# Performance work log

Hardware: AMD Instinct MI355X
Metric: run time of the kernel (lower is better)

The kernel has to match this reference:

```python
import jax, jax.numpy as jnp
import numpy as np

D_MODEL = 512
H = 8
DK = D_MODEL // H  # 64


def setup_inputs() -> dict:
    key = jax.random.key(0)
    ks = jax.random.split(key, 8)
    B, S = 2, 4096
    q = jax.random.normal(ks[0], (B, S, D_MODEL), dtype=jnp.float32)
    k = jax.random.normal(ks[1], (B, S, D_MODEL), dtype=jnp.float32)
    v = jax.random.normal(ks[2], (B, S, D_MODEL), dtype=jnp.float32)
    # per-head projection weights, torch nn.Linear layout [out, in], stacked over heads
    scale = 1.0 / np.sqrt(D_MODEL)
    Wq = jax.random.uniform(ks[3], (H, DK, D_MODEL), jnp.float32, -scale, scale)
    Wk = jax.random.uniform(ks[4], (H, DK, D_MODEL), jnp.float32, -scale, scale)
    Wv = jax.random.uniform(ks[5], (H, DK, D_MODEL), jnp.float32, -scale, scale)
    Wo = jax.random.uniform(ks[6], (D_MODEL, D_MODEL), jnp.float32, -scale, scale)
    # causal mask (True = keep), matches masked_fill(mask.logical_not(), -inf)
    mask = jnp.tril(jnp.ones((S, S), dtype=jnp.bool_))
    return {"q": q, "k": k, "v": v, "Wq": Wq, "Wk": Wk, "Wv": Wv, "Wo": Wo, "mask": mask}


def reference(q, k, v, Wq, Wk, Wv, Wo, mask):
    # per-head projections (stacked): x @ W^T for each head -> [B, H, S, DK]
    qh = jnp.einsum('bsd,hed->bhse', q, Wq)
    kh = jnp.einsum('bsd,hed->bhse', k, Wk)
    vh = jnp.einsum('bsd,hed->bhse', v, Wv)
    scaling = 1.0 / np.sqrt(DK)
    scores = jnp.einsum('bhse,bhte->bhst', qh, kh) * scaling  # [B,H,S,S]
    scores = jnp.where(mask, scores, -jnp.inf)
    attn = jax.nn.softmax(scores, axis=-1)
    heads = jnp.einsum('bhst,bhte->bhse', attn, vh)  # [B,H,S,DK]
    B, _, S, _ = heads.shape
    concat = jnp.transpose(heads, (0, 2, 1, 3)).reshape(B, S, D_MODEL)
    return concat @ Wo.T
```

## Files before the change

kernel.cpp:

```cpp
#include <hip/hip_runtime.h>
#include <hip/hip_bf16.h>
#include <math.h>

typedef __bf16 bf16_t;
typedef __bf16 bf16x8 __attribute__((ext_vector_type(8)));
typedef __bf16 bf16x4 __attribute__((ext_vector_type(4)));
typedef short short4v __attribute__((ext_vector_type(4)));
typedef float f32x4 __attribute__((ext_vector_type(4)));

__device__ __forceinline__ f32x4 mfma_k32(bf16x8 a, bf16x8 b, f32x4 c) {
    return __builtin_amdgcn_mfma_f32_16x16x32_bf16(a, b, c, 0, 0, 0);
}

__device__ __forceinline__ f32x4 mfma_k16(bf16x4 a, bf16x4 b, f32x4 c) {
#if __has_builtin(__builtin_amdgcn_mfma_f32_16x16x16_bf16)
    return __builtin_amdgcn_mfma_f32_16x16x16_bf16(a, b, c, 0, 0, 0);
#elif __has_builtin(__builtin_amdgcn_mfma_f32_16x16x16bf16_1k)
    short4v as, bs;
    __builtin_memcpy(&as, &a, 8);
    __builtin_memcpy(&bs, &b, 8);
    return __builtin_amdgcn_mfma_f32_16x16x16bf16_1k(as, bs, c, 0, 0, 0);
#else
    f32x4 d = c;
    asm volatile("v_mfma_f32_16x16x16_bf16 %0, %1, %2, %0" : "+v"(d) : "v"(a), "v"(b));
    return d;
#endif
}

__device__ __forceinline__ float fast_exp2(float x) {
#if __has_builtin(__builtin_amdgcn_exp2f)
    return __builtin_amdgcn_exp2f(x);
#else
    float r;
    asm("v_exp_f32 %0, %1" : "=v"(r) : "v"(x));
    return r;
#endif
}

__device__ __forceinline__ void async16(const bf16_t* g, __bf16* l) {
    __builtin_amdgcn_global_load_lds(
        (const __attribute__((address_space(1))) void*)g,
        (__attribute__((address_space(3))) void*)l, 16, 0, 0);
}

__device__ __forceinline__ int swz_col(int col, int row) {
    return (col & ~63) | ((((col >> 3) & 7) ^ (row & 7)) << 3) | (col & 7);
}

__global__ __launch_bounds__(256) void cvt_all(const float* __restrict__ q,
                                               const float* __restrict__ k,
                                               const float* __restrict__ v,
                                               const float* __restrict__ Wq,
                                               const float* __restrict__ Wk,
                                               const float* __restrict__ Wv,
                                               const float* __restrict__ Wo,
                                               bf16_t* __restrict__ qc,
                                               bf16_t* __restrict__ kc,
                                               bf16_t* __restrict__ vc,
                                               bf16_t* __restrict__ Wc) {
    const int bx = blockIdx.x;
    if (bx < 2048) {
        size_t i = ((size_t)bx * 256 + threadIdx.x) * 8;
        int row = (int)(i >> 9), col = (int)(i & 511);
        size_t di = (size_t)row * 512 + swz_col(col, row);
        float4 a0 = *(const float4*)(q + i), a1 = *(const float4*)(q + i + 4);
        float4 b0 = *(const float4*)(k + i), b1 = *(const float4*)(k + i + 4);
        float4 c0 = *(const float4*)(v + i), c1 = *(const float4*)(v + i + 4);
        bf16x8 qo, ko, vo;
        qo[0]=(__bf16)a0.x; qo[1]=(__bf16)a0.y; qo[2]=(__bf16)a0.z; qo[3]=(__bf16)a0.w;
        qo[4]=(__bf16)a1.x; qo[5]=(__bf16)a1.y; qo[6]=(__bf16)a1.z; qo[7]=(__bf16)a1.w;
        ko[0]=(__bf16)b0.x; ko[1]=(__bf16)b0.y; ko[2]=(__bf16)b0.z; ko[3]=(__bf16)b0.w;
        ko[4]=(__bf16)b1.x; ko[5]=(__bf16)b1.y; ko[6]=(__bf16)b1.z; ko[7]=(__bf16)b1.w;
        vo[0]=(__bf16)c0.x; vo[1]=(__bf16)c0.y; vo[2]=(__bf16)c0.z; vo[3]=(__bf16)c0.w;
        vo[4]=(__bf16)c1.x; vo[5]=(__bf16)c1.y; vo[6]=(__bf16)c1.z; vo[7]=(__bf16)c1.w;
        *(bf16x8*)(qc + di) = qo;
        *(bf16x8*)(kc + di) = ko;
        *(bf16x8*)(vc + di) = vo;
    } else {
        const int b2 = bx - 2048;
        const int m = b2 >> 7;
        const float* src = m == 0 ? Wq : m == 1 ? Wk : m == 2 ? Wv : Wo;
        const float sc = (m == 0) ? 0.125f * 1.44269504088896f : 1.0f;
        size_t i = ((size_t)(b2 & 127) * 256 + threadIdx.x) * 8;
        int row = (int)(i >> 9), col = (int)(i & 511);
        float4 a0 = *(const float4*)(src + i), a1 = *(const float4*)(src + i + 4);
        bf16x8 o;
        o[0]=(__bf16)(a0.x*sc); o[1]=(__bf16)(a0.y*sc); o[2]=(__bf16)(a0.z*sc); o[3]=(__bf16)(a0.w*sc);
        o[4]=(__bf16)(a1.x*sc); o[5]=(__bf16)(a1.y*sc); o[6]=(__bf16)(a1.z*sc); o[7]=(__bf16)(a1.w*sc);
        *(bf16x8*)(Wc + (size_t)m * 262144 + (size_t)row * 512 + swz_col(col, row)) = o;
    }
}

template<int MODE>
__device__ __forceinline__ void gemm128_body(const bf16_t* __restrict__ A,
                                             const bf16_t* __restrict__ B,
                                             void* __restrict__ outp,
                                             int m0, int n0) {
    __shared__ __bf16 Asm[128 * 64];
    __shared__ __bf16 Bsm[128 * 64];
    const int tid  = threadIdx.x;
    const int wave = tid >> 6;
    const int lane = tid & 63;
    const int quad = lane >> 4;
    const int l16  = lane & 15;
    const int swz  = l16 & 7;
    const int r8 = lane >> 3;
    const int c8 = (lane & 7) * 8;
    const int mrow0 = (wave & 1) * 64;
    const int ncol0 = (wave >> 1) * 64;

    f32x4 acc[4][4];
    for (int i = 0; i < 4; ++i)
        for (int j = 0; j < 4; ++j) acc[i][j] = (f32x4){0.f, 0.f, 0.f, 0.f};

    for (int kt = 0; kt < 512; kt += 64) {
        __syncthreads();
        for (int j = 0; j < 4; ++j) {
            async16(A + (size_t)(m0 + wave * 32 + j * 8 + r8) * 512 + kt + c8,
                    &Asm[(wave * 32 + j * 8) * 64]);
            async16(B + (size_t)(n0 + wave * 32 + j * 8 + r8) * 512 + kt + c8,
                    &Bsm[(wave * 32 + j * 8) * 64]);
        }
        __syncthreads();

        for (int ks = 0; ks < 2; ++ks) {
            bf16x8 af[4];
            for (int mt = 0; mt < 4; ++mt)
                af[mt] = *(const bf16x8*)&Asm[(mrow0 + mt * 16 + l16) * 64 + ((ks * 4 + quad) ^ swz) * 8];
            for (int nt = 0; nt < 4; ++nt) {
                bf16x8 bf = *(const bf16x8*)&Bsm[(ncol0 + nt * 16 + l16) * 64 + ((ks * 4 + quad) ^ swz) * 8];
                for (int mt = 0; mt < 4; ++mt)
                    acc[mt][nt] = mfma_k32(af[mt], bf, acc[mt][nt]);
            }
        }
    }

    if (MODE == 0) {
        bf16_t* out = (bf16_t*)outp;
        for (int nt = 0; nt < 4; ++nt) {
            int e = n0 + ncol0 + nt * 16 + l16;
            int h = e >> 6, el = e & 63;
            for (int mt = 0; mt < 4; ++mt)
                for (int r = 0; r < 4; ++r) {
                    int row = m0 + mrow0 + mt * 16 + quad * 4 + r;
                    int b = row >> 12, s = row & 4095;
                    int elp = (((el >> 3) ^ (row & 7)) << 3) | (el & 7);
                    out[(((size_t)(b * 8 + h)) * 4096 + s) * 64 + elp] = (bf16_t)acc[mt][nt][r];
                }
        }
    } else if (MODE == 1) {
        bf16_t* out = (bf16_t*)outp;
        for (int nt = 0; nt < 4; ++nt) {
            int s_g = n0 + ncol0 + nt * 16 + l16;
            int b = s_g >> 12;
            int sbase = (s_g & 4095) & ~63;
            int f = 16 * ((l16 >> 2) & 3) + 4 * nt + (l16 & 3);
            for (int mt = 0; mt < 4; ++mt)
                for (int r = 0; r < 4; ++r) {
                    int e_g = m0 + mrow0 + mt * 16 + quad * 4 + r;
                    int h = e_g >> 6, el = e_g & 63;
                    int col = sbase | ((((f >> 3) ^ (e_g & 7)) & 7) << 3) | (f & 7);
                    out[(((size_t)(b * 8 + h)) * 64 + el) * 4096 + col] = (bf16_t)acc[mt][nt][r];
                }
        }
    } else {
        float* out = (float*)outp;
        for (int nt = 0; nt < 4; ++nt) {
            int n = n0 + ncol0 + nt * 16 + l16;
            for (int mt = 0; mt < 4; ++mt)
                for (int r = 0; r < 4; ++r) {
                    int row = m0 + mrow0 + mt * 16 + quad * 4 + r;
                    out[(size_t)row * 512 + n] = acc[mt][nt][r];
                }
        }
    }
}

__global__ __launch_bounds__(256) void proj_fused(const bf16_t* __restrict__ xs,
                                                  const bf16_t* __restrict__ Wc,
                                                  bf16_t* __restrict__ qh,
                                                  bf16_t* __restrict__ kh,
                                                  bf16_t* __restrict__ vh) {
    const int z = blockIdx.z;
    const bf16_t* X = xs + (size_t)z * 4194304;
    const bf16_t* W = Wc + (size_t)z * 262144;
    if (z == 0)
        gemm128_body<0>(X, W, qh, blockIdx.x * 128, blockIdx.y * 128);
    else if (z == 1)
        gemm128_body<0>(X, W, kh, blockIdx.x * 128, blockIdx.y * 128);
    else
        gemm128_body<1>(W, X, vh, blockIdx.y * 128, blockIdx.x * 128);
}

__global__ __launch_bounds__(256) void gemm_final(const bf16_t* __restrict__ A,
                                                  const bf16_t* __restrict__ B,
                                                  float* __restrict__ out) {
    gemm128_body<2>(A, B, out, blockIdx.x * 128, blockIdx.y * 128);
}

__global__ __launch_bounds__(512, 4) void attn_kernel(const bf16_t* __restrict__ qh,
                                                      const bf16_t* __restrict__ kh,
                                                      const bf16_t* __restrict__ vh,
                                                      bf16_t* __restrict__ ao) {
    __shared__ __bf16 SM[32768];
    __bf16* KSM = &SM[0];
    __bf16* VSM = &SM[16384];
    float* Osc = (float*)SM;
    float* Lsc = (float*)&SM[24576];

    const int tid  = threadIdx.x;
    const int wave = tid >> 6;
    const int pp   = wave >> 1;
    const int wl   = wave & 1;
    const int lane = tid & 63;
    const int quad = lane >> 4;
    const int l16  = lane & 15;
    const int swz  = l16 & 7;
    const int bh   = blockIdx.y;
    const size_t base = (size_t)bh * 4096 * 64;
    const int r8 = lane >> 3;
    const int c8 = (lane & 7) * 8;
    const int b = bh >> 3, h = bh & 7;

    for (int leg = 0; leg < 2; ++leg) {
        const int qt = leg ? (63 - (int)blockIdx.x) : (int)blockIdx.x;
        const int q0 = qt * 64;

        bf16x8 qf[2][2];
        for (int g = 0; g < 2; ++g) {
            const bf16_t* qp = qh + base + (size_t)(q0 + wl * 32 + g * 16 + l16) * 64;
            qf[g][0] = *(const bf16x8*)(qp + ((quad ^ swz) * 8));
            qf[g][1] = *(const bf16x8*)(qp + (((4 + quad) ^ swz) * 8));
        }

        f32x4 o[2][4];
        for (int g = 0; g < 2; ++g)
            for (int i = 0; i < 4; ++i) o[g][i] = (f32x4){0.f, 0.f, 0.f, 0.f};
        float lsum[2] = {0.f, 0.f};

        const int iters = (qt + 4) >> 2;
        for (int it = 0; it < iters; ++it) {
            const int j0 = it * 256;
            const int koff = j0 + pp * 64 - q0;
            __syncthreads();
            if (koff <= 63) {
                for (int j = 0; j < 4; ++j) {
                    int row = wl * 32 + j * 8 + r8;
                    async16(kh + base + (size_t)(j0 + pp * 64 + row) * 64 + c8,
                            KSM + (pp * 64 + wl * 32 + j * 8) * 64);
                    async16(vh + (size_t)(bh * 64 + row) * 4096 + j0 + pp * 64 + c8,
                            VSM + (pp * 64 + wl * 32 + j * 8) * 64);
                }
            }
            __syncthreads();
            if (koff > wl * 32 + 31) continue;

            f32x4 st[2][4];
            for (int nt = 0; nt < 4; ++nt) {
                const __bf16* kr = KSM + (pp * 64 + nt * 16 + l16) * 64;
                bf16x8 kf0 = *(const bf16x8*)(kr + ((quad ^ swz) * 8));
                bf16x8 kf1 = *(const bf16x8*)(kr + (((4 + quad) ^ swz) * 8));
                for (int g = 0; g < 2; ++g) {
                    f32x4 zz = (f32x4){0.f, 0.f, 0.f, 0.f};
                    zz = mfma_k32(kf0, qf[g][0], zz);
                    zz = mfma_k32(kf1, qf[g][1], zz);
                    st[g][nt] = zz;
                }
            }

            bf16x4 pf[2][4];
            for (int g = 0; g < 2; ++g) {
                const int qb = wl * 32 + g * 16;
                if (koff + 63 <= qb) {
                    for (int nt = 0; nt < 4; ++nt)
                        for (int r = 0; r < 4; ++r) {
                            float p = fast_exp2(st[g][nt][r]);
                            lsum[g] += p;
                            pf[g][nt][r] = (bf16_t)p;
                        }
                } else {
                    const int qrow = qb + l16;
                    for (int nt = 0; nt < 4; ++nt)
                        for (int r = 0; r < 4; ++r) {
                            int key = nt * 16 + quad * 4 + r;
                            float p = (key + koff <= qrow) ? fast_exp2(st[g][nt][r]) : 0.f;
                            lsum[g] += p;
                            pf[g][nt][r] = (bf16_t)p;
                        }
                }
            }

            for (int dt = 0; dt < 4; ++dt)
                for (int kt2 = 0; kt2 < 2; ++kt2) {
                    bf16x8 vf = *(const bf16x8*)&VSM[(pp * 64 + dt * 16 + l16) * 64 + (((2 * quad + kt2) ^ swz) * 8)];
                    bf16x4 vlo = {vf[0], vf[1], vf[2], vf[3]};
                    bf16x4 vhi = {vf[4], vf[5], vf[6], vf[7]};
                    for (int g = 0; g < 2; ++g) {
                        o[g][dt] = mfma_k16(pf[g][2 * kt2], vlo, o[g][dt]);
                        o[g][dt] = mfma_k16(pf[g][2 * kt2 + 1], vhi, o[g][dt]);
                    }
                }
        }

        __syncthreads();
        if (pp != 0) {
            const int pi = pp - 1;
            for (int g = 0; g < 2; ++g) {
                float ls = lsum[g];
                ls += __shfl_xor(ls, 16);
                ls += __shfl_xor(ls, 32);
                const int qb = (pi * 2 + wl) * 32 + g * 16;
                Lsc[qb + l16] = ls;
                for (int dt = 0; dt < 4; ++dt)
                    for (int r = 0; r < 4; ++r)
                        Osc[(qb + quad * 4 + r) * 64 + dt * 16 + l16] = o[g][dt][r];
            }
        }
        __syncthreads();
        if (pp == 0) {
            for (int g = 0; g < 2; ++g) {
                float ls = lsum[g];
                ls += __shfl_xor(ls, 16);
                ls += __shfl_xor(ls, 32);
                const int qb = wl * 32 + g * 16;
                for (int pi = 0; pi < 3; ++pi)
                    ls += Lsc[(pi * 2 + wl) * 32 + g * 16 + l16];
                float linv[4];
                for (int r = 0; r < 4; ++r) linv[r] = 1.0f / __shfl(ls, quad * 4 + r);
                for (int r = 0; r < 4; ++r) {
                    int s_g = q0 + qb + quad * 4 + r;
                    size_t rowoff = ((size_t)(b * 4096 + s_g)) * 512;
                    for (int dt = 0; dt < 4; ++dt) {
                        float ov = o[g][dt][r];
                        for (int pi = 0; pi < 3; ++pi)
                            ov += Osc[((pi * 2 + wl) * 32 + g * 16 + quad * 4 + r) * 64 + dt * 16 + l16];
                        int el = dt * 16 + l16;
                        int elp = (((el >> 3) ^ (s_g & 7)) << 3) | (el & 7);
                        ao[rowoff + h * 64 + elp] = (bf16_t)(ov * linv[r]);
                    }
                }
            }
        }
    }
}

extern "C" void kernel_launch(void* const* d_in, const int* in_sizes, int n_in,
                              void* d_out, int out_size, void* d_ws, size_t ws_size,
                              hipStream_t stream) {
    const float* q  = (const float*)d_in[0];
    const float* k  = (const float*)d_in[1];
    const float* v  = (const float*)d_in[2];
    const float* Wq = (const float*)d_in[3];
    const float* Wk = (const float*)d_in[4];
    const float* Wv = (const float*)d_in[5];
    const float* Wo = (const float*)d_in[6];
    float* out = (float*)d_out;

    bf16_t* ws = (bf16_t*)d_ws;
    const size_t R = (size_t)8192 * 512;
    bf16_t* qc = ws;
    bf16_t* kc = ws + R;
    bf16_t* vc = ws + 2 * R;
    bf16_t* vh = ws + 3 * R;
    bf16_t* Wc = ws + 4 * R;
    bf16_t* qh = (bf16_t*)d_out;
    bf16_t* kh = (bf16_t*)d_out + R;
    bf16_t* ao = qc;

    cvt_all<<<dim3(2560), dim3(256), 0, stream>>>(q, k, v, Wq, Wk, Wv, Wo, qc, kc, vc, Wc);
    proj_fused<<<dim3(64, 4, 3), dim3(256), 0, stream>>>(ws, Wc, qh, kh, vh);
    attn_kernel<<<dim3(32, 16), dim3(512), 0, stream>>>(qh, kh, vh, ao);
    gemm_final<<<dim3(64, 4), dim3(256), 0, stream>>>(ao, Wc + 3 * 262144, out);
}
```

Measured before the change: 264.2 us.

## Split attention KV range across two blocks and add combine kernel

The attention kernel now uses 256-thread blocks, and each query tile's key range is split into two halves processed by separate blocks (split-K). Each block writes partial bf16 outputs and row sums to workspace. A new combine kernel sums the halves, normalizes and writes the swizzled output. Block ids are remapped so batch-heads interleave. This doubles the number of blocks, which should help occupancy and load balance across CUs. The cost is an extra launch, extra global traffic for the partials, and bf16 rounding of the partials before they are combined.

Result: faster. 253.9 us (-3.9%).

```diff
diff --git a/kernel.cpp b/kernel.cpp
--- a/kernel.cpp
+++ b/kernel.cpp
@@ -198,32 +198,39 @@
     gemm128_body<2>(A, B, out, blockIdx.x * 128, blockIdx.y * 128);
 }
 
-__global__ __launch_bounds__(512, 4) void attn_kernel(const bf16_t* __restrict__ qh,
+__global__ __launch_bounds__(256, 4) void attn_kernel(const bf16_t* __restrict__ qh,
                                                       const bf16_t* __restrict__ kh,
                                                       const bf16_t* __restrict__ vh,
-                                                      bf16_t* __restrict__ ao) {
-    __shared__ __bf16 SM[32768];
+                                                      bf16_t* __restrict__ Opart,
+                                                      float* __restrict__ Lpart) {
+    __shared__ __bf16 SM[16384];
     __bf16* KSM = &SM[0];
-    __bf16* VSM = &SM[16384];
+    __bf16* VSM = &SM[8192];
     float* Osc = (float*)SM;
-    float* Lsc = (float*)&SM[24576];
+    float* Lsc = (float*)&SM[8192];
+
+    const int id   = blockIdx.x;
+    const int bh   = ((id & 7) << 1) | ((id >> 3) & 1);
+    const int pair = (id >> 4) & 31;
+    const int z    = (id >> 9) & 1;
 
     const int tid  = threadIdx.x;
     const int wave = tid >> 6;
-    const int pp   = wave >> 1;
+    const int g2   = wave >> 1;
     const int wl   = wave & 1;
     const int lane = tid & 63;
     const int quad = lane >> 4;
     const int l16  = lane & 15;
     const int swz  = l16 & 7;
-    const int bh   = blockIdx.y;
     const size_t base = (size_t)bh * 4096 * 64;
     const int r8 = lane >> 3;
     const int c8 = (lane & 7) * 8;
-    const int b = bh >> 3, h = bh & 7;
+
+    bf16_t* Op = Opart + (size_t)z * 4194304;
+    float*  Lp = Lpart + z * 65536;
 
     for (int leg = 0; leg < 2; ++leg) {
-        const int qt = leg ? (63 - (int)blockIdx.x) : (int)blockIdx.x;
+        const int qt = leg ? (63 - pair) : pair;
         const int q0 = qt * 64;
 
         bf16x8 qf[2][2];
@@ -238,21 +245,26 @@
             for (int i = 0; i < 4; ++i) o[g][i] = (f32x4){0.f, 0.f, 0.f, 0.f};
         float lsum[2] = {0.f, 0.f};
 
-        const int iters = (qt + 4) >> 2;
-        for (int it = 0; it < iters; ++it) {
-            const int j0 = it * 256;
+        const int S  = (qt + 2) >> 1;
+        const int Sh = (S + 1) >> 1;
+        const int it0 = z ? Sh : 0;
+        const int it1 = z ? S : Sh;
+
+        for (int it = it0; it < it1; ++it) {
+            const int j0 = it * 128;
+            __syncthreads();
+            for (int p = 0; p < 2; ++p)
+                for (int j = 0; j < 2; ++j) {
+                    int row = wave * 16 + j * 8 + r8;
+                    async16(kh + base + (size_t)(j0 + p * 64 + row) * 64 + c8,
+                            KSM + (p * 64 + wave * 16 + j * 8) * 64);
+                    async16(vh + (size_t)(bh * 64 + row) * 4096 + j0 + p * 64 + c8,
+                            VSM + (p * 64 + wave * 16 + j * 8) * 64);
+                }
+            __syncthreads();
+
+            const int pp = g2;
             const int koff = j0 + pp * 64 - q0;
-            __syncthreads();
-            if (koff <= 63) {
-                for (int j = 0; j < 4; ++j) {
-                    int row = wl * 32 + j * 8 + r8;
-                    async16(kh + base + (size_t)(j0 + pp * 64 + row) * 64 + c8,
-                            KSM + (pp * 64 + wl * 32 + j * 8) * 64);
-                    async16(vh + (size_t)(bh * 64 + row) * 4096 + j0 + pp * 64 + c8,
-                            VSM + (pp * 64 + wl * 32 + j * 8) * 64);
-                }
-            }
-            __syncthreads();
             if (koff > wl * 32 + 31) continue;
 
             f32x4 st[2][4];
@@ -303,44 +315,76 @@
         }
 
         __syncthreads();
-        if (pp != 0) {
-            const int pi = pp - 1;
-            for (int g = 0; g < 2; ++g) {
-                float ls = lsum[g];
-                ls += __shfl_xor(ls, 16);
-                ls += __shfl_xor(ls, 32);
-                const int qb = (pi * 2 + wl) * 32 + g * 16;
-                Lsc[qb + l16] = ls;
-                for (int dt = 0; dt < 4; ++dt)
-                    for (int r = 0; r < 4; ++r)
-                        Osc[(qb + quad * 4 + r) * 64 + dt * 16 + l16] = o[g][dt][r];
-            }
-        }
-        __syncthreads();
-        if (pp == 0) {
+        if (g2 == 1) {
             for (int g = 0; g < 2; ++g) {
                 float ls = lsum[g];
                 ls += __shfl_xor(ls, 16);
                 ls += __shfl_xor(ls, 32);
                 const int qb = wl * 32 + g * 16;
-                for (int pi = 0; pi < 3; ++pi)
-                    ls += Lsc[(pi * 2 + wl) * 32 + g * 16 + l16];
-                float linv[4];
-                for (int r = 0; r < 4; ++r) linv[r] = 1.0f / __shfl(ls, quad * 4 + r);
-                for (int r = 0; r < 4; ++r) {
-                    int s_g = q0 + qb + quad * 4 + r;
-                    size_t rowoff = ((size_t)(b * 4096 + s_g)) * 512;
-                    for (int dt = 0; dt < 4; ++dt) {
-                        float ov = o[g][dt][r];
-                        for (int pi = 0; pi < 3; ++pi)
-                            ov += Osc[((pi * 2 + wl) * 32 + g * 16 + quad * 4 + r) * 64 + dt * 16 + l16];
-                        int el = dt * 16 + l16;
-                        int elp = (((el >> 3) ^ (s_g & 7)) << 3) | (el & 7);
-                        ao[rowoff + h * 64 + elp] = (bf16_t)(ov * linv[r]);
+                Lsc[qb + l16] = ls;
+                for (int dt = 0; dt < 4; ++dt)
+                    for (int r = 0; r < 4; ++r)
+                        Osc[(qb + quad * 4 + r) * 64 + dt * 16 + l16] = o[g][dt][r];
+            }
+        }
+        __syncthreads();
+        if (g2 == 0) {
+            for (int g = 0; g < 2; ++g) {
+                float ls = lsum[g];
+                ls += __shfl_xor(ls, 16);
+                ls += __shfl_xor(ls, 32);
+                const int qb = wl * 32 + g * 16;
+                ls += Lsc[qb + l16];
+                Lsc[qb + l16] = ls;
+                for (int dt = 0; dt < 4; ++dt)
+                    for (int r = 0; r < 4; ++r) {
+                        int idx = (qb + quad * 4 + r) * 64 + dt * 16 + l16;
+                        Osc[idx] = o[g][dt][r] + Osc[idx];
                     }
-                }
-            }
-        }
+            }
+        }
+        __syncthreads();
+        {
+            const int q  = tid >> 2;
+            const int e0 = (tid & 3) * 16;
+            bf16x8 w0, w1;
+            for (int i = 0; i < 8; ++i) {
+                w0[i] = (bf16_t)Osc[q * 64 + e0 + i];
+                w1[i] = (bf16_t)Osc[q * 64 + e0 + 8 + i];
+            }
+            size_t slot = ((size_t)(bh * 64 + qt)) * 4096 + q * 64 + e0;
+            *(bf16x8*)&Op[slot]     = w0;
+            *(bf16x8*)&Op[slot + 8] = w1;
+            if (tid < 64) Lp[(bh * 64 + qt) * 64 + tid] = Lsc[tid];
+        }
+    }
+}
+
+__global__ __launch_bounds__(256) void attn_combine(const bf16_t* __restrict__ Opart,
+                                                    const float* __restrict__ Lpart,
+                                                    bf16_t* __restrict__ ao) {
+    const int unit = blockIdx.x * 4 + (threadIdx.x >> 6);
+    const int q    = threadIdx.x & 63;
+    const int bh = unit >> 6, qt = unit & 63;
+    const int b = bh >> 3, h = bh & 7;
+    const size_t ro = (size_t)unit * 4096 + q * 64;
+
+    float o[64];
+    const bf16x8* p0 = (const bf16x8*)(Opart + ro);
+    const bf16x8* p1 = (const bf16x8*)(Opart + 4194304 + ro);
+    for (int c = 0; c < 8; ++c) {
+        bf16x8 a = p0[c], bb = p1[c];
+        for (int i = 0; i < 8; ++i) o[c * 8 + i] = (float)a[i] + (float)bb[i];
+    }
+    float L = Lpart[unit * 64 + q] + Lpart[65536 + unit * 64 + q];
+    float inv = 1.0f / L;
+    int s_g = qt * 64 + q, sw = s_g & 7;
+    size_t rowoff = ((size_t)(b * 4096 + s_g)) * 512 + h * 64;
+    for (int c = 0; c < 8; ++c) {
+        int e0 = (c ^ sw) * 8;
+        bf16x8 w;
+        for (int i = 0; i < 8; ++i) w[i] = (bf16_t)(o[e0 + i] * inv);
+        *(bf16x8*)&ao[rowoff + c * 8] = w;
     }
 }
 
@@ -363,12 +407,14 @@
     bf16_t* vc = ws + 2 * R;
     bf16_t* vh = ws + 3 * R;
     bf16_t* Wc = ws + 4 * R;
+    float*  Lp = (float*)(ws + 4 * R + 1048576);
     bf16_t* qh = (bf16_t*)d_out;
     bf16_t* kh = (bf16_t*)d_out + R;
     bf16_t* ao = qc;
 
     cvt_all<<<dim3(2560), dim3(256), 0, stream>>>(q, k, v, Wq, Wk, Wv, Wo, qc, kc, vc, Wc);
     proj_fused<<<dim3(64, 4, 3), dim3(256), 0, stream>>>(ws, Wc, qh, kh, vh);
-    attn_kernel<<<dim3(32, 16), dim3(512), 0, stream>>>(qh, kh, vh, ao);
+    attn_kernel<<<dim3(1024), dim3(256), 0, stream>>>(qh, kh, vh, kc, Lp);
+    attn_combine<<<dim3(256), dim3(256), 0, stream>>>(kc, Lp, ao);
     gemm_final<<<dim3(64, 4), dim3(256), 0, stream>>>(ao, Wc + 3 * 262144, out);
 }
```
